# Kernel tuning notes

Measured on AMD Instinct MI355X. Metric: run time of the kernel, lower is better.

The kernel has to match this reference:

```python
import jax, jax.numpy as jnp
import numpy as np

IN_FEATS = 128
OUT_FEATS = 128
ASSIGN_DIM = 256
BATCH_SIZE = 8
N = 12288
E = 196608
CPG = ASSIGN_DIM // BATCH_SIZE  # clusters per graph (block width of the mask)


def setup_inputs() -> dict:
    key = jax.random.key(0)
    ks = jax.random.split(key, 6)
    x = jax.random.normal(ks[0], (N, IN_FEATS), dtype=jnp.float32)
    edge_index = jax.random.randint(ks[1], (2, E), 0, N, dtype=jnp.int32)
    batch = jnp.sort(jax.random.randint(ks[2], (N,), 0, BATCH_SIZE, dtype=jnp.int32))
    s = 1.0 / np.sqrt(2 * IN_FEATS)
    W_embd = jax.random.uniform(ks[3], (2 * IN_FEATS, OUT_FEATS), minval=-s, maxval=s, dtype=jnp.float32)
    b_embd = jnp.zeros((OUT_FEATS,), jnp.float32)
    W_pool = jax.random.uniform(ks[4], (2 * IN_FEATS, ASSIGN_DIM), minval=-s, maxval=s, dtype=jnp.float32)
    b_pool = jnp.zeros((ASSIGN_DIM,), jnp.float32)
    return dict(x=x, edge_index=edge_index, batch=batch,
                W_embd=W_embd, b_embd=b_embd, W_pool=W_pool, b_pool=b_pool)


def _sage_conv(x, src, dst, W, b):
    # GraphSAGE mean aggregator, concat([self, agg]) @ W + b, row L2-normalize.
    agg = jax.ops.segment_sum(x[src], dst, num_segments=N)                 # [N, F]
    deg = jax.ops.segment_sum(jnp.ones((E,), x.dtype), dst, num_segments=N)
    agg = agg / jnp.maximum(deg, 1.0)[:, None]
    h = jnp.concatenate([x, agg], axis=-1) @ W + b
    return h / jnp.maximum(jnp.linalg.norm(h, axis=-1, keepdims=True), 1e-12)


def _masked_softmax_nonme(m, mask):
    # memory_efficient=False branch of masked_softmax
    r = jax.nn.softmax(m * mask, axis=-1)
    r = r * mask
    return r / (r.sum(axis=-1, keepdims=True) + 1e-13)


def reference(x, edge_index, batch, W_embd, b_embd, W_pool, b_pool):
    src, dst = edge_index[0], edge_index[1]
    embed = _sage_conv(x, src, dst, W_embd, b_embd)    # [N, out_feats]
    pooled = _sage_conv(x, src, dst, W_pool, b_pool)   # [N, assign_dim]

    # block-diagonal mask: node i sees the assign columns of its own graph
    col_graph = jnp.arange(ASSIGN_DIM, dtype=batch.dtype) // CPG
    mask = (batch[:, None] == col_graph[None, :]).astype(pooled.dtype)  # [N, assign_dim]

    result = _masked_softmax_nonme(pooled, mask)        # [N, assign_dim]
    h = result.T @ embed                                # [assign_dim, out_feats]

    # adjacency coarsening: S^T A S with edge weights = 1 (duplicates sum)
    Ar = jax.ops.segment_sum(result[dst], src, num_segments=N)  # A @ result
    adj_new = result.T @ Ar                              # [assign_dim, assign_dim]

    # link prediction loss: ||A_dense - S S^T||_F / N^2 (dense NxN, as original)
    A_dense = jnp.zeros((N, N), result.dtype).at[src, dst].add(1.0)
    adj_loss = jnp.linalg.norm(A_dense - result @ result.T) / (N ** 2)

    # entropy loss over Categorical(probs=mask): uniform over each block
    p = mask / mask.sum(axis=-1, keepdims=True)
    ent = -jnp.sum(jnp.where(p > 0, p * jnp.log(jnp.where(p > 0, p, 1.0)), 0.0), axis=-1)
    entropy_loss = ent.sum()

    return adj_new, h, adj_loss, entropy_loss
```

## Files before the change

kernel.cpp:

```cpp
#include <hip/hip_runtime.h>
#include <math.h>

#define NN 12288
#define EE 196608
#define FIN 128
#define AD 256
#define NG 8
#define ACH 32
#define GCH 16
#define BCAP 128
#define CLP 404
#define APITCH 8256
#define HPITCH 4160
#define GPITCH 1088

using short8 = __attribute__((ext_vector_type(8))) short;
using floatx4 = __attribute__((ext_vector_type(4))) float;

__device__ __forceinline__ unsigned short f2bf(float f) {
  union { float f; unsigned u; } v; v.f = f;
  unsigned r = v.u + 0x7FFFu + ((v.u >> 16) & 1u);
  return (unsigned short)(r >> 16);
}


__global__ __launch_bounds__(256) void k_setup(const float* __restrict__ We, const float* __restrict__ be,
    const float* __restrict__ Wp, const float* __restrict__ bp, const int* __restrict__ batch,
    unsigned* cnt_dst, unsigned* cnt_src, double* acc, unsigned* done,
    unsigned short* __restrict__ WTb, float* __restrict__ bcat, int* __restrict__ gstart) {
  unsigned i = blockIdx.x * 256u + threadIdx.x;
  if (i < 384u * 256u) {
    unsigned n = i >> 8, k = i & 255u;
    float v = (n < 128u) ? We[k * 128u + n] : Wp[k * 256u + (n - 128u)];
    WTb[i] = f2bf(v);
  }
  if (i < 384u) bcat[i] = (i < 128u) ? be[i] : bp[i - 128u];
  if (i < NN) { cnt_dst[i] = 0u; cnt_src[i] = 0u; }
  if (i < 3u) acc[i] = 0.0;
  if (i == 3u) *done = 0u;
  if (i <= NG) {
    int g = (int)i, lo = 0, hi = NN;
    while (lo < hi) { int mid = (lo + hi) >> 1; if (batch[mid] < g) lo = mid + 1; else hi = mid; }
    gstart[g] = lo;
  }
}


__global__ __launch_bounds__(256) void k_edgeB(const int* __restrict__ src, const int* __restrict__ dst,
    unsigned* cnt_dst, unsigned* cnt_src, int* __restrict__ bdst, int* __restrict__ bsrc) {
  unsigned e = blockIdx.x * 256u + threadIdx.x;
  if (e >= EE) return;
  int s = src[e], d = dst[e];
  unsigned p = atomicAdd(&cnt_dst[d], 1u);
  if (p < BCAP) bdst[(size_t)d * BCAP + p] = s;
  unsigned q = atomicAdd(&cnt_src[s], 1u);
  if (q < BCAP) bsrc[(size_t)s * BCAP + q] = d;
}


__global__ __launch_bounds__(256) void k_dupagg(const float* __restrict__ x,
    const unsigned* __restrict__ cnt_dst, const int* __restrict__ bdst,
    unsigned short* __restrict__ Zb, unsigned* __restrict__ dup_part) {
  int node = blockIdx.x * 4 + (threadIdx.x >> 6);
  int lane = threadIdx.x & 63;
  unsigned deg = cnt_dst[node];
  unsigned m = deg < BCAP ? deg : BCAP;
  const int* bk = bdst + (size_t)node * BCAP;
  unsigned cnt = 0;
  for (unsigned i0 = 0; i0 < m; i0 += 64) {
    int si = (i0 + lane < m) ? bk[i0 + lane] : -1;
    for (unsigned j = 0; j < m; j++) {
      int sj = bk[j];
      cnt += (si == sj) ? 1u : 0u;
    }
  }
#pragma unroll
  for (int o = 32; o >= 1; o >>= 1) cnt += __shfl_xor(cnt, o, 64);
  if (lane == 0) dup_part[node] = cnt;
  const float2* x2 = (const float2*)x;
  float ax = 0.f, ay = 0.f;
  for (unsigned k = 0; k < m; k++) {
    int s = bk[k];
    float2 v = x2[(size_t)s * 64 + lane];
    ax += v.x; ay += v.y;
  }
  float inv = 1.f / fmaxf((float)deg, 1.f);
  float2 sv = x2[(size_t)node * 64 + lane];
  ushort2* Zb2 = (ushort2*)Zb;
  ushort2 a; a.x = f2bf(sv.x); a.y = f2bf(sv.y);
  ushort2 mm; mm.x = f2bf(ax * inv); mm.y = f2bf(ay * inv);
  Zb2[(size_t)node * 128 + lane] = a;
  Zb2[(size_t)node * 128 + 64 + lane] = mm;
}


__global__ __launch_bounds__(256) void k_gemmnorm(const unsigned short* __restrict__ Zb,
    const unsigned short* __restrict__ WTb, const float* __restrict__ bcat,
    const int* __restrict__ batch, float* __restrict__ embed, float* __restrict__ Rc) {
  __shared__ unsigned short Bl[24 * 512];
  __shared__ unsigned short Al[2 * 512];
  __shared__ float Cl[32 * CLP];
  int t = threadIdx.x;
  int gm = blockIdx.x * 32;
  int w = t >> 6, l = t & 63;

  floatx4 acc[2][6] = {};

  for (int kc = 0; kc < 8; kc++) {
    __syncthreads();
#pragma unroll
    for (int i = 0; i < 7; i++) {
      int p = t + i * 256;
      if (p < 1536) {
        int n = p >> 2, quad = p & 3;
        uint4 v = *(const uint4*)&WTb[(size_t)n * 256 + kc * 32 + quad * 8];
        *(uint4*)&Bl[(n >> 4) * 512 + ((n & 15) + 16 * quad) * 8] = v;
      } else if (p < 1664) {
        int p2 = p - 1536;
        int m = p2 >> 2, quad = p2 & 3;
        uint4 v = *(const uint4*)&Zb[(size_t)(gm + m) * 256 + kc * 32 + quad * 8];
        *(uint4*)&Al[(m >> 4) * 512 + ((m & 15) + 16 * quad) * 8] = v;
      }
    }
    __syncthreads();
    short8 a0 = *(const short8*)&Al[l * 8];
    short8 a1 = *(const short8*)&Al[512 + l * 8];
#pragma unroll
    for (int c6 = 0; c6 < 6; c6++) {
      short8 b = *(const short8*)&Bl[(w * 6 + c6) * 512 + l * 8];
      acc[0][c6] = __builtin_amdgcn_mfma_f32_16x16x32_bf16(a0, b, acc[0][c6], 0, 0, 0);
      acc[1][c6] = __builtin_amdgcn_mfma_f32_16x16x32_bf16(a1, b, acc[1][c6], 0, 0, 0);
    }
  }

  int col16 = l & 15, quad = l >> 4;
#pragma unroll
  for (int s = 0; s < 2; s++) {
#pragma unroll
    for (int c6 = 0; c6 < 6; c6++) {
      int colg = (w * 6 + c6) * 16 + col16;
      float bias = bcat[colg];
#pragma unroll
      for (int r = 0; r < 4; r++)
        Cl[(s * 16 + quad * 4 + r) * CLP + colg] = acc[s][c6][r] + bias;
    }
  }
  __syncthreads();

  for (int rr = 0; rr < 8; rr++) {
    int row = w * 8 + rr;
    int node = gm + row;
    const float* crow = &Cl[row * CLP];
    float v0 = crow[l], v1 = crow[64 + l];
    float ss = v0 * v0 + v1 * v1;
#pragma unroll
    for (int o = 32; o >= 1; o >>= 1) ss += __shfl_xor(ss, o, 64);
    float inv = 1.f / fmaxf(sqrtf(ss), 1e-12f);
    embed[(size_t)node * 128 + l] = v0 * inv;
    embed[(size_t)node * 128 + 64 + l] = v1 * inv;
    float4 p = *(const float4*)&crow[128 + 4 * l];
    float ss2 = p.x * p.x + p.y * p.y + p.z * p.z + p.w * p.w;
#pragma unroll
    for (int o = 32; o >= 1; o >>= 1) ss2 += __shfl_xor(ss2, o, 64);
    float inv2 = 1.f / fmaxf(sqrtf(ss2), 1e-12f);
    p.x *= inv2; p.y *= inv2; p.z *= inv2; p.w *= inv2;
    int g = batch[node];
    if ((l >> 3) == g) {
      float m = fmaxf(fmaxf(p.x, p.y), fmaxf(p.z, p.w));
#pragma unroll
      for (int o = 1; o <= 4; o <<= 1) m = fmaxf(m, __shfl_xor(m, o, 64));
      float e0 = expf(p.x - m), e1 = expf(p.y - m), e2 = expf(p.z - m), e3 = expf(p.w - m);
      float sum = e0 + e1 + e2 + e3;
#pragma unroll
      for (int o = 1; o <= 4; o <<= 1) sum += __shfl_xor(sum, o, 64);
      float r = 1.f / sum;
      float4 q; q.x = e0 * r; q.y = e1 * r; q.z = e2 * r; q.w = e3 * r;
      *(float4*)&Rc[(size_t)node * 32 + 4 * (l - g * 8)] = q;
    }
  }
}


__global__ __launch_bounds__(256) void k_ar(const float* __restrict__ Rc,
    const unsigned* __restrict__ cnt_src, const int* __restrict__ bsrc,
    const int* __restrict__ batch, float* __restrict__ Ar) {
  int node = blockIdx.x * 4 + (threadIdx.x >> 6);
  int lane = threadIdx.x & 63;
  int lg = lane >> 3, li = lane & 7;
  unsigned deg = cnt_src[node];
  unsigned m = deg < BCAP ? deg : BCAP;
  const int* bk = bsrc + (size_t)node * BCAP;
  float4 acc = {0.f, 0.f, 0.f, 0.f};
  const float4* R4 = (const float4*)Rc;
  for (unsigned k = 0; k < m; k++) {
    int d = bk[k];
    int g = batch[d];
    if (lg == g) {
      float4 r = R4[(size_t)d * 8 + li];
      acc.x += r.x; acc.y += r.y; acc.z += r.z; acc.w += r.w;
    }
  }
  ((float4*)Ar)[(size_t)node * 64 + lane] = acc;
}


__global__ __launch_bounds__(256) void k_big3(const float* __restrict__ Rc,
    const float* __restrict__ embed, const float* __restrict__ Ar, const int* __restrict__ gstart,
    float* __restrict__ part_h, float* __restrict__ part_adj, float* __restrict__ Gpart) {
  int role = blockIdx.z;
  int g = blockIdx.x, ch = blockIdx.y;
  if (role == 2 && ch >= GCH) return;
  int s0 = gstart[g], e0 = gstart[g + 1];
  int nch = (role == 2) ? GCH : ACH;
  int per = (e0 - s0 + nch - 1) / nch;
  int i0 = s0 + ch * per;
  int i1 = i0 + per; if (i1 > e0) i1 = e0;
  int t = threadIdx.x;
  __shared__ float rcs[128][32];

  if (role == 0) {
    int f4 = t & 31, c1g = t >> 5;
    float4 acc[4] = {};
    const float4* E4 = (const float4*)embed;
    for (int ib = i0; ib < i1; ib += 64) {
      int cnt = i1 - ib; if (cnt > 64) cnt = 64;
      __syncthreads();
      const float4* s4 = (const float4*)(Rc + (size_t)ib * 32);
      for (int idx = t; idx < cnt * 8; idx += 256) ((float4*)rcs)[idx] = s4[idx];
      __syncthreads();
      for (int n = 0; n < cnt; n++) {
        float4 e4 = E4[(size_t)(ib + n) * 32 + f4];
        float4 r = *(const float4*)&rcs[n][c1g * 4];
        float rv[4] = {r.x, r.y, r.z, r.w};
#pragma unroll
        for (int j = 0; j < 4; j++) {
          acc[j].x += rv[j] * e4.x; acc[j].y += rv[j] * e4.y;
          acc[j].z += rv[j] * e4.z; acc[j].w += rv[j] * e4.w;
        }
      }
    }
    float* p = part_h + (size_t)(g * ACH + ch) * HPITCH;
#pragma unroll
    for (int j = 0; j < 4; j++)
      *(float4*)&p[(c1g * 4 + j) * 128 + f4 * 4] = acc[j];
  } else if (role == 1) {
    int c2q = t & 63, c1g = t >> 6;
    float4 acc[8] = {};
    const float4* Ar4 = (const float4*)Ar;
    for (int ib = i0; ib < i1; ib += 64) {
      int cnt = i1 - ib; if (cnt > 64) cnt = 64;
      __syncthreads();
      const float4* s4 = (const float4*)(Rc + (size_t)ib * 32);
      for (int idx = t; idx < cnt * 8; idx += 256) ((float4*)rcs)[idx] = s4[idx];
      __syncthreads();
      for (int n = 0; n < cnt; n++) {
        float4 a4 = Ar4[(size_t)(ib + n) * 64 + c2q];
        float4 r0 = *(const float4*)&rcs[n][c1g * 8];
        float4 r1 = *(const float4*)&rcs[n][c1g * 8 + 4];
        float rv[8] = {r0.x, r0.y, r0.z, r0.w, r1.x, r1.y, r1.z, r1.w};
#pragma unroll
        for (int j = 0; j < 8; j++) {
          acc[j].x += rv[j] * a4.x; acc[j].y += rv[j] * a4.y;
          acc[j].z += rv[j] * a4.z; acc[j].w += rv[j] * a4.w;
        }
      }
    }
    float* p = part_adj + (size_t)(g * ACH + ch) * APITCH;
#pragma unroll
    for (int j = 0; j < 8; j++)
      *(float4*)&p[(c1g * 8 + j) * 256 + c2q * 4] = acc[j];
  } else {
    int c2q = t & 7, c1 = t >> 3;
    float4 acc = {};
    for (int ib = i0; ib < i1; ib += 128) {
      int cnt = i1 - ib; if (cnt > 128) cnt = 128;
      __syncthreads();
      const float4* s4 = (const float4*)(Rc + (size_t)ib * 32);
      for (int idx = t; idx < cnt * 8; idx += 256) ((float4*)rcs)[idx] = s4[idx];
      __syncthreads();
      for (int n = 0; n < cnt; n++) {
        float4 r2 = *(const float4*)&rcs[n][c2q * 4];
        float r1 = rcs[n][c1];
        acc.x += r1 * r2.x; acc.y += r1 * r2.y; acc.z += r1 * r2.z; acc.w += r1 * r2.w;
      }
    }
    *(float4*)&Gpart[(size_t)(g * GCH + ch) * GPITCH + c1 * 32 + c2q * 4] = acc;
  }
}


__global__ __launch_bounds__(256) void k_red3(const float* __restrict__ part_adj,
    const float* __restrict__ part_h, const float* __restrict__ Gpart,
    const unsigned* __restrict__ dup_part,
    float* __restrict__ outa, float* __restrict__ outh,
    double* __restrict__ acc, unsigned* __restrict__ done, float* __restrict__ out) {
  int b = blockIdx.x, t = threadIdx.x;
  int lane = t & 63;
  if (b < 256) {
    int i = b * 256 + t;
    int g = i >> 13, off = i & 8191;
    const float* base = part_adj + (size_t)g * ACH * APITCH + off;
    float s = 0.f;
#pragma unroll
    for (int ch = 0; ch < ACH; ch++) s += base[(size_t)ch * APITCH];
    outa[i] = s;
    if (t == b) atomicAdd(&acc[0], (double)s);
  } else if (b < 384) {
    int j = (b - 256) * 256 + t;
    int g = j >> 12, off = j & 4095;
    const float* base = part_h + (size_t)g * ACH * HPITCH + off;
    float s = 0.f;
#pragma unroll
    for (int ch = 0; ch < ACH; ch++) s += base[(size_t)ch * HPITCH];
    outh[j] = s;
  } else if (b < 416) {
    int j = (b - 384) * 256 + t;
    int g = j >> 10, off = j & 1023;
    const float* base = Gpart + (size_t)g * GCH * GPITCH + off;
    float s = 0.f;
#pragma unroll
    for (int ch = 0; ch < GCH; ch++) s += base[(size_t)ch * GPITCH];
    double g2 = (double)s * (double)s;
#pragma unroll
    for (int o = 32; o >= 1; o >>= 1) g2 += __shfl_xor(g2, o, 64);
    if (lane == 0) atomicAdd(&acc[1], g2);
  } else {
    int j = (b - 416) * 256 + t;
    double a2 = (double)dup_part[j];
#pragma unroll
    for (int o = 32; o >= 1; o >>= 1) a2 += __shfl_xor(a2, o, 64);
    if (lane == 0) atomicAdd(&acc[2], a2);
  }
  __syncthreads();
  if (t == 0) {
    unsigned prev = atomicAdd(done, 1u);
    if (prev == gridDim.x - 1) {
      double trf = atomicAdd(&acc[0], 0.0);
      double g2f = atomicAdd(&acc[1], 0.0);
      double a2f = atomicAdd(&acc[2], 0.0);
      double val = a2f - 2.0 * trf + g2f;
      if (val < 0.0) val = 0.0;
      out[98304] = (float)(sqrt(val) / ((double)NN * (double)NN));
      out[98305] = (float)((double)NN * log(32.0));
    }
  }
}


extern "C" void kernel_launch(void* const* d_in, const int* in_sizes, int n_in,
                              void* d_out, int out_size, void* d_ws, size_t ws_size,
                              hipStream_t stream) {
  const float* x = (const float*)d_in[0];
  const int* ei = (const int*)d_in[1];
  const int* src = ei;
  const int* dst = ei + EE;
  const int* batch = (const int*)d_in[2];
  const float* Wemb = (const float*)d_in[3];
  const float* bemb = (const float*)d_in[4];
  const float* Wpool = (const float*)d_in[5];
  const float* bpool = (const float*)d_in[6];
  float* out = (float*)d_out;

  char* w = (char*)d_ws;
  size_t off = 0;
  auto A = [&](size_t bytes) -> char* {
    char* p = w + off;
    off += (bytes + 255) & ~(size_t)255;
    return p;
  };
  unsigned* cnt_dst = (unsigned*)A(NN * 4);
  unsigned* cnt_src = (unsigned*)A(NN * 4);
  int* bdst = (int*)A((size_t)NN * BCAP * 4);
  int* bsrc = (int*)A((size_t)NN * BCAP * 4);
  int* gstart = (int*)A(64);
  unsigned* dup_part = (unsigned*)A(NN * 4);
  double* acc = (double*)A(3 * 8);
  unsigned* done = (unsigned*)A(4);
  unsigned short* Zb = (unsigned short*)A((size_t)NN * 256 * 2);
  float* embed = (float*)A((size_t)NN * FIN * 4);
  float* Rc = (float*)A((size_t)NN * 32 * 4);
  float* Ar = (float*)A((size_t)NN * AD * 4);
  unsigned short* WTb = (unsigned short*)A(384 * 256 * 2);
  float* bcat = (float*)A(384 * 4);
  float* part_h = (float*)A((size_t)8 * ACH * HPITCH * 4);
  float* part_adj = (float*)A((size_t)8 * ACH * APITCH * 4);
  float* Gpart = (float*)A((size_t)8 * GCH * GPITCH * 4);
  (void)ws_size; (void)in_sizes; (void)n_in; (void)out_size;

  k_setup<<<dim3(384), dim3(256), 0, stream>>>(Wemb, bemb, Wpool, bpool, batch,
      cnt_dst, cnt_src, acc, done, WTb, bcat, gstart);
  k_edgeB<<<dim3(EE / 256), dim3(256), 0, stream>>>(src, dst, cnt_dst, cnt_src, bdst, bsrc);
  k_dupagg<<<dim3(NN / 4), dim3(256), 0, stream>>>(x, cnt_dst, bdst, Zb, dup_part);
  k_gemmnorm<<<dim3(NN / 32), dim3(256), 0, stream>>>(Zb, WTb, bcat, batch, embed, Rc);
  k_ar<<<dim3(NN / 4), dim3(256), 0, stream>>>(Rc, cnt_src, bsrc, batch, Ar);
  k_big3<<<dim3(8, ACH, 3), dim3(256), 0, stream>>>(Rc, embed, Ar, gstart, part_h, part_adj, Gpart);
  k_red3<<<dim3(464), dim3(256), 0, stream>>>(part_adj, part_h, Gpart, dup_part,
      out, out + 65536, acc, done, out);
}
```

Measured before the change: 204.6 us.

## Restructure SAGE GEMM epilogue in registers and pack graph id into src buckets

The fused GEMM+normalize kernel now gives each wave 16 rows across all 384 output columns. Row norms and the per-graph softmax are computed directly from MFMA accumulators with 16-lane shuffles, which removes the large LDS staging buffer and its extra barrier. The block also covers 64 rows instead of 32, halving the grid. Separately, the edge bucketing kernel packs the destination's graph id into the high bits of each source-bucket entry, so the Ar gather no longer does a dependent load of batch[d] per edge. The trade-off is 96 accumulator registers per thread, which may lower occupancy, plus fewer blocks in flight.

```diff
diff --git a/kernel.cpp b/kernel.cpp
--- a/kernel.cpp
+++ b/kernel.cpp
@@ -9,7 +9,6 @@
 #define ACH 32
 #define GCH 16
 #define BCAP 128
-#define CLP 404
 #define APITCH 8256
 #define HPITCH 4160
 #define GPITCH 1088
@@ -47,14 +46,16 @@
 
 
 __global__ __launch_bounds__(256) void k_edgeB(const int* __restrict__ src, const int* __restrict__ dst,
+    const int* __restrict__ batch,
     unsigned* cnt_dst, unsigned* cnt_src, int* __restrict__ bdst, int* __restrict__ bsrc) {
   unsigned e = blockIdx.x * 256u + threadIdx.x;
   if (e >= EE) return;
   int s = src[e], d = dst[e];
   unsigned p = atomicAdd(&cnt_dst[d], 1u);
   if (p < BCAP) bdst[(size_t)d * BCAP + p] = s;
+  int gd = batch[d];
   unsigned q = atomicAdd(&cnt_src[s], 1u);
-  if (q < BCAP) bsrc[(size_t)s * BCAP + q] = d;
+  if (q < BCAP) bsrc[(size_t)s * BCAP + q] = (gd << 14) | d;
 }
 
 
@@ -98,13 +99,12 @@
     const unsigned short* __restrict__ WTb, const float* __restrict__ bcat,
     const int* __restrict__ batch, float* __restrict__ embed, float* __restrict__ Rc) {
   __shared__ unsigned short Bl[24 * 512];
-  __shared__ unsigned short Al[2 * 512];
-  __shared__ float Cl[32 * CLP];
+  __shared__ unsigned short Al[4 * 512];
   int t = threadIdx.x;
-  int gm = blockIdx.x * 32;
+  int gm = blockIdx.x * 64;
   int w = t >> 6, l = t & 63;
 
-  floatx4 acc[2][6] = {};
+  floatx4 acc[24] = {};
 
   for (int kc = 0; kc < 8; kc++) {
     __syncthreads();
@@ -115,7 +115,7 @@
         int n = p >> 2, quad = p & 3;
         uint4 v = *(const uint4*)&WTb[(size_t)n * 256 + kc * 32 + quad * 8];
         *(uint4*)&Bl[(n >> 4) * 512 + ((n & 15) + 16 * quad) * 8] = v;
-      } else if (p < 1664) {
+      } else {
         int p2 = p - 1536;
         int m = p2 >> 2, quad = p2 & 3;
         uint4 v = *(const uint4*)&Zb[(size_t)(gm + m) * 256 + kc * 32 + quad * 8];
@@ -123,67 +123,65 @@
       }
     }
     __syncthreads();
-    short8 a0 = *(const short8*)&Al[l * 8];
-    short8 a1 = *(const short8*)&Al[512 + l * 8];
-#pragma unroll
-    for (int c6 = 0; c6 < 6; c6++) {
-      short8 b = *(const short8*)&Bl[(w * 6 + c6) * 512 + l * 8];
-      acc[0][c6] = __builtin_amdgcn_mfma_f32_16x16x32_bf16(a0, b, acc[0][c6], 0, 0, 0);
-      acc[1][c6] = __builtin_amdgcn_mfma_f32_16x16x32_bf16(a1, b, acc[1][c6], 0, 0, 0);
+    short8 a = *(const short8*)&Al[w * 512 + l * 8];
+#pragma unroll
+    for (int tt = 0; tt < 24; tt++) {
+      short8 b = *(const short8*)&Bl[tt * 512 + l * 8];
+      acc[tt] = __builtin_amdgcn_mfma_f32_16x16x32_bf16(a, b, acc[tt], 0, 0, 0);
     }
   }
 
   int col16 = l & 15, quad = l >> 4;
 #pragma unroll
-  for (int s = 0; s < 2; s++) {
-#pragma unroll
-    for (int c6 = 0; c6 < 6; c6++) {
-      int colg = (w * 6 + c6) * 16 + col16;
-      float bias = bcat[colg];
-#pragma unroll
-      for (int r = 0; r < 4; r++)
-        Cl[(s * 16 + quad * 4 + r) * CLP + colg] = acc[s][c6][r] + bias;
-    }
-  }
-  __syncthreads();
-
-  for (int rr = 0; rr < 8; rr++) {
-    int row = w * 8 + rr;
-    int node = gm + row;
-    const float* crow = &Cl[row * CLP];
-    float v0 = crow[l], v1 = crow[64 + l];
-    float ss = v0 * v0 + v1 * v1;
-#pragma unroll
-    for (int o = 32; o >= 1; o >>= 1) ss += __shfl_xor(ss, o, 64);
+  for (int tt = 0; tt < 24; tt++) {
+    float b = bcat[tt * 16 + col16];
+    acc[tt][0] += b; acc[tt][1] += b; acc[tt][2] += b; acc[tt][3] += b;
+  }
+
+#pragma unroll
+  for (int r = 0; r < 4; r++) {
+    int node = gm + w * 16 + quad * 4 + r;
+    float ss = 0.f;
+#pragma unroll
+    for (int tt = 0; tt < 8; tt++) { float v = acc[tt][r]; ss += v * v; }
+#pragma unroll
+    for (int o = 8; o >= 1; o >>= 1) ss += __shfl_xor(ss, o, 64);
     float inv = 1.f / fmaxf(sqrtf(ss), 1e-12f);
-    embed[(size_t)node * 128 + l] = v0 * inv;
-    embed[(size_t)node * 128 + 64 + l] = v1 * inv;
-    float4 p = *(const float4*)&crow[128 + 4 * l];
-    float ss2 = p.x * p.x + p.y * p.y + p.z * p.z + p.w * p.w;
-#pragma unroll
-    for (int o = 32; o >= 1; o >>= 1) ss2 += __shfl_xor(ss2, o, 64);
+#pragma unroll
+    for (int tt = 0; tt < 8; tt++)
+      embed[(size_t)node * 128 + tt * 16 + col16] = acc[tt][r] * inv;
+    float ss2 = 0.f;
+#pragma unroll
+    for (int tt = 8; tt < 24; tt++) { float v = acc[tt][r]; ss2 += v * v; }
+#pragma unroll
+    for (int o = 8; o >= 1; o >>= 1) ss2 += __shfl_xor(ss2, o, 64);
     float inv2 = 1.f / fmaxf(sqrtf(ss2), 1e-12f);
-    p.x *= inv2; p.y *= inv2; p.z *= inv2; p.w *= inv2;
     int g = batch[node];
-    if ((l >> 3) == g) {
-      float m = fmaxf(fmaxf(p.x, p.y), fmaxf(p.z, p.w));
-#pragma unroll
-      for (int o = 1; o <= 4; o <<= 1) m = fmaxf(m, __shfl_xor(m, o, 64));
-      float e0 = expf(p.x - m), e1 = expf(p.y - m), e2 = expf(p.z - m), e3 = expf(p.w - m);
-      float sum = e0 + e1 + e2 + e3;
-#pragma unroll
-      for (int o = 1; o <= 4; o <<= 1) sum += __shfl_xor(sum, o, 64);
-      float r = 1.f / sum;
-      float4 q; q.x = e0 * r; q.y = e1 * r; q.z = e2 * r; q.w = e3 * r;
-      *(float4*)&Rc[(size_t)node * 32 + 4 * (l - g * 8)] = q;
-    }
+    float v0 = 0.f, v1 = 0.f;
+#pragma unroll
+    for (int tg = 0; tg < 8; tg++) {
+      bool sel = (tg == g);
+      v0 = sel ? acc[8 + 2 * tg][r] : v0;
+      v1 = sel ? acc[9 + 2 * tg][r] : v1;
+    }
+    v0 *= inv2; v1 *= inv2;
+    float mx = fmaxf(v0, v1);
+#pragma unroll
+    for (int o = 8; o >= 1; o >>= 1) mx = fmaxf(mx, __shfl_xor(mx, o, 64));
+    float e0 = expf(v0 - mx), e1 = expf(v1 - mx);
+    float sm = e0 + e1;
+#pragma unroll
+    for (int o = 8; o >= 1; o >>= 1) sm += __shfl_xor(sm, o, 64);
+    float rr = 1.f / sm;
+    Rc[(size_t)node * 32 + col16] = e0 * rr;
+    Rc[(size_t)node * 32 + 16 + col16] = e1 * rr;
   }
 }
 
 
 __global__ __launch_bounds__(256) void k_ar(const float* __restrict__ Rc,
     const unsigned* __restrict__ cnt_src, const int* __restrict__ bsrc,
-    const int* __restrict__ batch, float* __restrict__ Ar) {
+    float* __restrict__ Ar) {
   int node = blockIdx.x * 4 + (threadIdx.x >> 6);
   int lane = threadIdx.x & 63;
   int lg = lane >> 3, li = lane & 7;
@@ -193,8 +191,8 @@
   float4 acc = {0.f, 0.f, 0.f, 0.f};
   const float4* R4 = (const float4*)Rc;
   for (unsigned k = 0; k < m; k++) {
-    int d = bk[k];
-    int g = batch[d];
+    int packed = bk[k];
+    int d = packed & 16383, g = packed >> 14;
     if (lg == g) {
       float4 r = R4[(size_t)d * 8 + li];
       acc.x += r.x; acc.y += r.y; acc.z += r.z; acc.w += r.w;
@@ -389,10 +387,10 @@
 
   k_setup<<<dim3(384), dim3(256), 0, stream>>>(Wemb, bemb, Wpool, bpool, batch,
       cnt_dst, cnt_src, acc, done, WTb, bcat, gstart);
-  k_edgeB<<<dim3(EE / 256), dim3(256), 0, stream>>>(src, dst, cnt_dst, cnt_src, bdst, bsrc);
+  k_edgeB<<<dim3(EE / 256), dim3(256), 0, stream>>>(src, dst, batch, cnt_dst, cnt_src, bdst, bsrc);
   k_dupagg<<<dim3(NN / 4), dim3(256), 0, stream>>>(x, cnt_dst, bdst, Zb, dup_part);
-  k_gemmnorm<<<dim3(NN / 32), dim3(256), 0, stream>>>(Zb, WTb, bcat, batch, embed, Rc);
-  k_ar<<<dim3(NN / 4), dim3(256), 0, stream>>>(Rc, cnt_src, bsrc, batch, Ar);
+  k_gemmnorm<<<dim3(NN / 64), dim3(256), 0, stream>>>(Zb, WTb, bcat, batch, embed, Rc);
+  k_ar<<<dim3(NN / 4), dim3(256), 0, stream>>>(Rc, cnt_src, bsrc, Ar);
   k_big3<<<dim3(8, ACH, 3), dim3(256), 0, stream>>>(Rc, embed, Ar, gstart, part_h, part_adj, Gpart);
   k_red3<<<dim3(464), dim3(256), 0, stream>>>(part_adj, part_h, Gpart, dup_part,
       out, out + 65536, acc, done, out);
```

Result: faster. 196.5 us (-4.0%).
